# Kernel optimization log

Hardware: AMD Instinct MI355X
Metric: run time of the kernel (lower is better)

The kernel has to match this reference:

```python
import jax, jax.numpy as jnp
import numpy as np

B, Nm, No, D = 32, 256, 1024, 1024
HID, C, K = 2048, 200, 3
EPS = 0.001  # label smoothing
ALPHA = 0.3  # scene-feature fusion weight


def setup_inputs() -> dict:
    key = jax.random.key(0)
    ks = jax.random.split(key, 9)
    return {
        "scene_feat": jax.random.normal(ks[0], (B, No, D), jnp.float32),
        "motion_feat": jax.random.normal(ks[1], (B, Nm, D), jnp.float32),
        "scene_loc": jax.random.normal(ks[2], (B, No, 2), jnp.float32),
        "motion_loc": jax.random.normal(ks[3], (B, Nm, 2), jnp.float32),
        "label": jax.random.randint(ks[4], (B,), 0, C),
        "Wp": jax.random.normal(ks[5], (D, HID), jnp.float32) * 0.02,
        "bp": jnp.zeros((HID,), jnp.float32),
        "Wc": jax.random.normal(ks[6], (HID, C), jnp.float32) * 0.02,
        "bc": jnp.zeros((C,), jnp.float32),
    }


def reference(scene_feat, motion_feat, scene_loc, motion_loc, label, Wp, bp, Wc, bc):
    # pairwise L2 distances: [B, Nm, No]
    diff = motion_loc[:, :, None, :] - scene_loc[:, None, :, :]
    dist = jnp.linalg.norm(diff, axis=-1)
    # k smallest distances -> nearest scene indices [B, Nm, K]
    _, idx = jax.lax.top_k(-dist, K)
    # gather nearest scene features per motion token: [B, Nm, K, D]
    nearest = jax.vmap(lambda sf, ix: sf[ix])(scene_feat, idx)
    fused = motion_feat + ALPHA * nearest.mean(axis=2)  # [B, Nm, D]
    x = fused.mean(axis=1)                              # [B, D]
    x = jax.nn.gelu(x @ Wp + bp, approximate=False)     # exact GELU (torch default)
    logit = x @ Wc + bc                                 # [B, C]
    # cross entropy with label smoothing (torch semantics)
    logp = jax.nn.log_softmax(logit, axis=-1)
    nll = -jnp.take_along_axis(logp, label[:, None], axis=1)[:, 0]
    smooth = -logp.mean(axis=-1)
    loss = jnp.mean((1.0 - EPS) * nll + EPS * smooth)
    return logit, loss
```

## Files before the change

### kernel.cpp

```cpp
#include <hip/hip_runtime.h>
#include <hip/hip_bf16.h>
#include <math.h>

#define BB_ 32
#define NM_ 256
#define NO_ 1024
#define DD_ 1024
#define HID_ 2048
#define CC_ 200
#define KK_ 3
#define EPS_ 0.001f
#define ALPHA_ 0.3f
#define NSEG_ 32
#define NSEG2_ 64

typedef unsigned long long u64;

__device__ __forceinline__ void ins3_u64(u64 k, u64& k0, u64& k1, u64& k2) {
    bool lt0 = k < k0, lt1 = k < k1, lt2 = k < k2;
    k2 = lt1 ? k1 : (lt2 ? k : k2);
    k1 = lt0 ? k0 : (lt1 ? k : k1);
    k0 = lt0 ? k : k0;
}

__global__ __launch_bounds__(256) void knn_idx_kernel(
        const float* __restrict__ scene_loc, const float* __restrict__ motion_loc,
        int* __restrict__ idx_buf) {
    int bx = blockIdx.x;
    int b = bx >> 5;
    int mc = bx & 31;
    __shared__ float slx[NO_], sly[NO_];
    const float2* sl = (const float2*)(scene_loc + (size_t)b * NO_ * 2);
    for (int i = threadIdx.x; i < NO_; i += 256) {
        float2 v = sl[i];
        slx[i] = v.x;
        sly[i] = v.y;
    }
    __syncthreads();

    int m = mc * 8 + (threadIdx.x >> 5);
    int lane = threadIdx.x & 31;
    float2 ml = ((const float2*)(motion_loc + (size_t)b * NM_ * 2))[m];

    u64 k0 = ~0ull, k1 = ~0ull, k2 = ~0ull;
    #pragma unroll 4
    for (int j = 0; j < 32; ++j) {
        int o = lane + (j << 5);
        float dx = ml.x - slx[o];
        float dy = ml.y - sly[o];
        float dist = __fsqrt_rn(__fadd_rn(__fmul_rn(dx, dx), __fmul_rn(dy, dy)));
        u64 k = ((u64)__float_as_uint(dist) << 32) | (unsigned)o;
        ins3_u64(k, k0, k1, k2);
    }
    #pragma unroll
    for (int mask = 1; mask <= 16; mask <<= 1) {
        u64 e0 = __shfl_xor(k0, mask);
        u64 e1 = __shfl_xor(k1, mask);
        u64 e2 = __shfl_xor(k2, mask);
        ins3_u64(e0, k0, k1, k2);
        ins3_u64(e1, k0, k1, k2);
        ins3_u64(e2, k0, k1, k2);
    }
    if (lane == 0) {
        int base = (b * NM_ + m) * 3;
        idx_buf[base]     = (int)(k0 & 0xFFFFFFFFu);
        idx_buf[base + 1] = (int)(k1 & 0xFFFFFFFFu);
        idx_buf[base + 2] = (int)(k2 & 0xFFFFFFFFu);
    }
}

__global__ __launch_bounds__(256) void prep_kernel(
        const int* __restrict__ idx_buf, int* __restrict__ mcnt,
        int* __restrict__ ol, float* __restrict__ wl) {
    int b = blockIdx.x;
    int t = threadIdx.x;
    const float wsc = ALPHA_ / (float)(NM_ * KK_);
    __shared__ int cnt[NO_];
    for (int i = t; i < NO_; i += 256) cnt[i] = 0;
    __syncthreads();
    const int* ib = idx_buf + b * NM_ * KK_;
    for (int i = t; i < NM_ * KK_; i += 256)
        atomicAdd(&cnt[ib[i]], 1);
    __syncthreads();

    int w = t >> 6;
    int lane = t & 63;
    #pragma unroll
    for (int si = 0; si < 8; ++si) {
        int s = w * 8 + si;
        if (lane < 32) {
            int o = s + (lane << 5);
            int c = cnt[o];
            unsigned long long ball = __ballot(c != 0);
            int pos = __popcll(ball & ((1ull << lane) - 1ull));
            if (c != 0) {
                ol[((size_t)b * NSEG_ + s) * 32 + pos] = o;
                wl[((size_t)b * NSEG_ + s) * 32 + pos] = wsc * (float)c;
            }
            if (lane == 0) mcnt[b * NSEG_ + s] = __popcll(ball);
        }
    }
}

__global__ __launch_bounds__(256) void fuse_mean_kernel(
        const float* __restrict__ scene_feat, const float* __restrict__ motion_feat,
        const int* __restrict__ mcnt, const int* __restrict__ ol,
        const float* __restrict__ wl, float* __restrict__ xpart) {
    int bx = blockIdx.x;
    int b = bx >> 6;
    int s2 = bx & 63;
    int s = s2 >> 1, h = s2 & 1;
    int t = threadIdx.x;
    const float wmot = 1.0f / (float)NM_;

    __shared__ float wls[32];
    __shared__ int ols[32];
    __shared__ int msh;
    if (t == 0) msh = mcnt[b * NSEG_ + s];
    if (t < 32) {
        ols[t] = ol[((size_t)b * NSEG_ + s) * 32 + t];
        wls[t] = wl[((size_t)b * NSEG_ + s) * 32 + t];
    }
    __syncthreads();
    int m = msh;

    float4 acc = make_float4(0.f, 0.f, 0.f, 0.f);
    const float4* mf = (const float4*)(motion_feat + (size_t)b * NM_ * DD_);
    #pragma unroll
    for (int j = 0; j < 4; ++j) {
        int r = s + (((j << 1) + h) << 5);
        float4 v = mf[(size_t)r * 256 + t];
        acc.x = fmaf(wmot, v.x, acc.x);
        acc.y = fmaf(wmot, v.y, acc.y);
        acc.z = fmaf(wmot, v.z, acc.z);
        acc.w = fmaf(wmot, v.w, acc.w);
    }
    const float4* sf = (const float4*)(scene_feat + (size_t)b * NO_ * DD_);
    #pragma unroll 4
    for (int i = h; i < m; i += 2) {
        float w = wls[i];
        float4 v = sf[(size_t)ols[i] * 256 + t];
        acc.x = fmaf(w, v.x, acc.x);
        acc.y = fmaf(w, v.y, acc.y);
        acc.z = fmaf(w, v.z, acc.z);
        acc.w = fmaf(w, v.w, acc.w);
    }
    ((float4*)(xpart + ((size_t)s2 * BB_ + b) * DD_))[t] = acc;
}

__global__ __launch_bounds__(256) void xsum_kernel(
        const float* __restrict__ xpart, float* __restrict__ x) {
    int b = blockIdx.x;
    int t = threadIdx.x;
    float4 acc = make_float4(0.f, 0.f, 0.f, 0.f);
    #pragma unroll 8
    for (int s = 0; s < NSEG2_; ++s) {
        float4 v = ((const float4*)(xpart + ((size_t)s * BB_ + b) * DD_))[t];
        acc.x += v.x; acc.y += v.y; acc.z += v.z; acc.w += v.w;
    }
    ((float4*)(x + (size_t)b * DD_))[t] = acc;
}

__global__ __launch_bounds__(256) void fc1_kernel(
        const float* __restrict__ x, const float* __restrict__ Wp,
        float* __restrict__ hpart) {
    int jc = blockIdx.x & 7;
    int dc = blockIdx.x >> 3;
    int t = threadIdx.x;
    int j = jc * 256 + t;

    __shared__ float xs[BB_ * 32];
    {
        int bb = t >> 3;
        int dl4 = t & 7;
        float4 v = ((const float4*)(x + (size_t)bb * DD_ + dc * 32))[dl4];
        ((float4*)xs)[t] = v;
    }
    __syncthreads();

    float acc[BB_];
    #pragma unroll
    for (int bb = 0; bb < BB_; ++bb) acc[bb] = 0.f;

    int d0 = dc * 32;
    for (int dl = 0; dl < 32; ++dl) {
        float w = Wp[(size_t)(d0 + dl) * HID_ + j];
        #pragma unroll
        for (int bb = 0; bb < BB_; ++bb)
            acc[bb] = fmaf(xs[bb * 32 + dl], w, acc[bb]);
    }
    #pragma unroll
    for (int bb = 0; bb < BB_; ++bb)
        hpart[((size_t)dc * BB_ + bb) * HID_ + j] = acc[bb];
}

__global__ __launch_bounds__(256) void fc2_partial_kernel(
        const float* __restrict__ hpart, const float* __restrict__ bp,
        const float* __restrict__ Wc, float* __restrict__ lpart) {
    int bx = blockIdx.x;
    int b = bx & 31;
    int kc = bx >> 5;
    int t = threadIdx.x;
    __shared__ float hs[256];

    int k = kc * 256 + t;
    float sum = bp[k];
    #pragma unroll
    for (int dcc = 0; dcc < 32; ++dcc)
        sum += hpart[((size_t)dcc * BB_ + b) * HID_ + k];
    hs[t] = 0.5f * sum * (1.0f + erff(sum * 0.70710678118654752f));
    __syncthreads();

    if (t < CC_) {
        float acc0 = 0.f, acc1 = 0.f;
        const float* wc = Wc + (size_t)kc * 256 * CC_ + t;
        #pragma unroll 8
        for (int k2 = 0; k2 < 256; k2 += 2) {
            acc0 = fmaf(hs[k2],     wc[(size_t)k2 * CC_],       acc0);
            acc1 = fmaf(hs[k2 + 1], wc[(size_t)(k2 + 1) * CC_], acc1);
        }
        lpart[((size_t)kc * BB_ + b) * CC_ + t] = acc0 + acc1;
    }
}

__global__ __launch_bounds__(256) void logits_loss_kernel(
        const float* __restrict__ lpart, const float* __restrict__ bc,
        const int* __restrict__ label, float* __restrict__ out) {
    int t = threadIdx.x;
    __shared__ float slog[BB_ * CC_];
    __shared__ float lossb[BB_];

    for (int idx = t; idx < BB_ * CC_; idx += 256) {
        int b = idx / CC_;
        int c = idx - b * CC_;
        float acc = bc[c];
        #pragma unroll
        for (int kc = 0; kc < 8; ++kc)
            acc += lpart[((size_t)kc * BB_ + b) * CC_ + c];
        slog[idx] = acc;
        out[idx] = acc;
    }
    __syncthreads();

    int b = t >> 3;
    int lane = t & 7;
    float v[25];
    float m = -INFINITY, ssum = 0.f;
    #pragma unroll
    for (int i = 0; i < 25; ++i) {
        float x = slog[b * CC_ + lane + i * 8];
        v[i] = x;
        m = fmaxf(m, x);
        ssum += x;
    }
    for (int mask = 1; mask < 8; mask <<= 1) m = fmaxf(m, __shfl_xor(m, mask));
    for (int mask = 1; mask < 8; mask <<= 1) ssum += __shfl_xor(ssum, mask);
    float e = 0.f;
    #pragma unroll
    for (int i = 0; i < 25; ++i) e += expf(v[i] - m);
    for (int mask = 1; mask < 8; mask <<= 1) e += __shfl_xor(e, mask);
    float logZ = m + logf(e);

    if (lane == 0) {
        float nll = logZ - slog[b * CC_ + label[b]];
        float smooth = logZ - ssum * (1.0f / (float)CC_);
        lossb[b] = (1.0f - EPS_) * nll + EPS_ * smooth;
    }
    __syncthreads();
    if (t == 0) {
        float s = 0.f;
        for (int i = 0; i < BB_; ++i) s += lossb[i];
        out[BB_ * CC_] = s * (1.0f / (float)BB_);
    }
}

extern "C" void kernel_launch(void* const* d_in, const int* in_sizes, int n_in,
                              void* d_out, int out_size, void* d_ws, size_t ws_size,
                              hipStream_t stream) {
    const float* scene_feat  = (const float*)d_in[0];
    const float* motion_feat = (const float*)d_in[1];
    const float* scene_loc   = (const float*)d_in[2];
    const float* motion_loc  = (const float*)d_in[3];
    const int*   label       = (const int*)d_in[4];
    const float* Wp          = (const float*)d_in[5];
    const float* bp          = (const float*)d_in[6];
    const float* Wc          = (const float*)d_in[7];
    const float* bc          = (const float*)d_in[8];
    float* out = (float*)d_out;

    char* ws = (char*)d_ws;
    int*   idx_buf = (int*)ws;
    int*   mcnt    = (int*)(ws + (128 << 10));
    int*   ol      = (int*)(ws + (256 << 10));
    float* wl      = (float*)(ws + (512 << 10));
    float* xpart   = (float*)(ws + (1 << 20));
    float* x       = (float*)(ws + (10 << 20));
    float* hpart   = (float*)(ws + (16 << 20));
    float* lpart   = (float*)(ws + (32 << 20));

    knn_idx_kernel<<<BB_ * 32, 256, 0, stream>>>(scene_loc, motion_loc, idx_buf);
    prep_kernel<<<BB_, 256, 0, stream>>>(idx_buf, mcnt, ol, wl);
    fuse_mean_kernel<<<BB_ * NSEG2_, 256, 0, stream>>>(scene_feat, motion_feat, mcnt, ol, wl, xpart);
    xsum_kernel<<<BB_, 256, 0, stream>>>(xpart, x);
    fc1_kernel<<<256, 256, 0, stream>>>(x, Wp, hpart);
    fc2_partial_kernel<<<256, 256, 0, stream>>>(hpart, bp, Wc, lpart);
    logits_loss_kernel<<<1, 256, 0, stream>>>(lpart, bc, label, out);
}
```

Measured before the change: 76.65 us.

## Overlap motion-feature mean with KNN search and split logits/loss kernels

```diff
diff --git a/kernel.cpp b/kernel.cpp
--- a/kernel.cpp
+++ b/kernel.cpp
@@ -23,49 +23,71 @@
     k0 = lt0 ? k : k0;
 }
 
-__global__ __launch_bounds__(256) void knn_idx_kernel(
+__global__ __launch_bounds__(256) void knn_motion_kernel(
         const float* __restrict__ scene_loc, const float* __restrict__ motion_loc,
-        int* __restrict__ idx_buf) {
+        const float* __restrict__ motion_feat,
+        int* __restrict__ idx_buf, float* __restrict__ xm) {
     int bx = blockIdx.x;
-    int b = bx >> 5;
-    int mc = bx & 31;
-    __shared__ float slx[NO_], sly[NO_];
-    const float2* sl = (const float2*)(scene_loc + (size_t)b * NO_ * 2);
-    for (int i = threadIdx.x; i < NO_; i += 256) {
-        float2 v = sl[i];
-        slx[i] = v.x;
-        sly[i] = v.y;
-    }
-    __syncthreads();
-
-    int m = mc * 8 + (threadIdx.x >> 5);
-    int lane = threadIdx.x & 31;
-    float2 ml = ((const float2*)(motion_loc + (size_t)b * NM_ * 2))[m];
-
-    u64 k0 = ~0ull, k1 = ~0ull, k2 = ~0ull;
-    #pragma unroll 4
-    for (int j = 0; j < 32; ++j) {
-        int o = lane + (j << 5);
-        float dx = ml.x - slx[o];
-        float dy = ml.y - sly[o];
-        float dist = __fsqrt_rn(__fadd_rn(__fmul_rn(dx, dx), __fmul_rn(dy, dy)));
-        u64 k = ((u64)__float_as_uint(dist) << 32) | (unsigned)o;
-        ins3_u64(k, k0, k1, k2);
-    }
-    #pragma unroll
-    for (int mask = 1; mask <= 16; mask <<= 1) {
-        u64 e0 = __shfl_xor(k0, mask);
-        u64 e1 = __shfl_xor(k1, mask);
-        u64 e2 = __shfl_xor(k2, mask);
-        ins3_u64(e0, k0, k1, k2);
-        ins3_u64(e1, k0, k1, k2);
-        ins3_u64(e2, k0, k1, k2);
-    }
-    if (lane == 0) {
-        int base = (b * NM_ + m) * 3;
-        idx_buf[base]     = (int)(k0 & 0xFFFFFFFFu);
-        idx_buf[base + 1] = (int)(k1 & 0xFFFFFFFFu);
-        idx_buf[base + 2] = (int)(k2 & 0xFFFFFFFFu);
+    if (bx < BB_ * 32) {
+        int b = bx >> 5;
+        int mc = bx & 31;
+        __shared__ float slx[NO_], sly[NO_];
+        const float2* sl = (const float2*)(scene_loc + (size_t)b * NO_ * 2);
+        for (int i = threadIdx.x; i < NO_; i += 256) {
+            float2 v = sl[i];
+            slx[i] = v.x;
+            sly[i] = v.y;
+        }
+        __syncthreads();
+
+        int m = mc * 8 + (threadIdx.x >> 5);
+        int lane = threadIdx.x & 31;
+        float2 ml = ((const float2*)(motion_loc + (size_t)b * NM_ * 2))[m];
+
+        u64 k0 = ~0ull, k1 = ~0ull, k2 = ~0ull;
+        #pragma unroll 4
+        for (int j = 0; j < 32; ++j) {
+            int o = lane + (j << 5);
+            float dx = ml.x - slx[o];
+            float dy = ml.y - sly[o];
+            float dist = __fsqrt_rn(__fadd_rn(__fmul_rn(dx, dx), __fmul_rn(dy, dy)));
+            u64 k = ((u64)__float_as_uint(dist) << 32) | (unsigned)o;
+            ins3_u64(k, k0, k1, k2);
+        }
+        #pragma unroll
+        for (int mask = 1; mask <= 16; mask <<= 1) {
+            u64 e0 = __shfl_xor(k0, mask);
+            u64 e1 = __shfl_xor(k1, mask);
+            u64 e2 = __shfl_xor(k2, mask);
+            ins3_u64(e0, k0, k1, k2);
+            ins3_u64(e1, k0, k1, k2);
+            ins3_u64(e2, k0, k1, k2);
+        }
+        if (lane == 0) {
+            int base = (b * NM_ + m) * 3;
+            idx_buf[base]     = (int)(k0 & 0xFFFFFFFFu);
+            idx_buf[base + 1] = (int)(k1 & 0xFFFFFFFFu);
+            idx_buf[base + 2] = (int)(k2 & 0xFFFFFFFFu);
+        }
+    } else {
+        int m2 = bx - BB_ * 32;
+        int b = m2 >> 6;
+        int s2 = m2 & 63;
+        int s = s2 >> 1, h = s2 & 1;
+        int t = threadIdx.x;
+        const float wmot = 1.0f / (float)NM_;
+        float4 acc = make_float4(0.f, 0.f, 0.f, 0.f);
+        const float4* mf = (const float4*)(motion_feat + (size_t)b * NM_ * DD_);
+        #pragma unroll
+        for (int j = 0; j < 4; ++j) {
+            int r = s + (((j << 1) + h) << 5);
+            float4 v = mf[(size_t)r * 256 + t];
+            acc.x = fmaf(wmot, v.x, acc.x);
+            acc.y = fmaf(wmot, v.y, acc.y);
+            acc.z = fmaf(wmot, v.z, acc.z);
+            acc.w = fmaf(wmot, v.w, acc.w);
+        }
+        ((float4*)(xm + ((size_t)s2 * BB_ + b) * DD_))[t] = acc;
     }
 }
 
@@ -102,16 +124,15 @@
     }
 }
 
-__global__ __launch_bounds__(256) void fuse_mean_kernel(
-        const float* __restrict__ scene_feat, const float* __restrict__ motion_feat,
-        const int* __restrict__ mcnt, const int* __restrict__ ol,
-        const float* __restrict__ wl, float* __restrict__ xpart) {
+__global__ __launch_bounds__(256) void scene_fuse_kernel(
+        const float* __restrict__ scene_feat, const int* __restrict__ mcnt,
+        const int* __restrict__ ol, const float* __restrict__ wl,
+        float* __restrict__ xsc) {
     int bx = blockIdx.x;
     int b = bx >> 6;
     int s2 = bx & 63;
     int s = s2 >> 1, h = s2 & 1;
     int t = threadIdx.x;
-    const float wmot = 1.0f / (float)NM_;
 
     __shared__ float wls[32];
     __shared__ int ols[32];
@@ -125,16 +146,6 @@
     int m = msh;
 
     float4 acc = make_float4(0.f, 0.f, 0.f, 0.f);
-    const float4* mf = (const float4*)(motion_feat + (size_t)b * NM_ * DD_);
-    #pragma unroll
-    for (int j = 0; j < 4; ++j) {
-        int r = s + (((j << 1) + h) << 5);
-        float4 v = mf[(size_t)r * 256 + t];
-        acc.x = fmaf(wmot, v.x, acc.x);
-        acc.y = fmaf(wmot, v.y, acc.y);
-        acc.z = fmaf(wmot, v.z, acc.z);
-        acc.w = fmaf(wmot, v.w, acc.w);
-    }
     const float4* sf = (const float4*)(scene_feat + (size_t)b * NO_ * DD_);
     #pragma unroll 4
     for (int i = h; i < m; i += 2) {
@@ -145,17 +156,23 @@
         acc.z = fmaf(w, v.z, acc.z);
         acc.w = fmaf(w, v.w, acc.w);
     }
-    ((float4*)(xpart + ((size_t)s2 * BB_ + b) * DD_))[t] = acc;
+    ((float4*)(xsc + ((size_t)s2 * BB_ + b) * DD_))[t] = acc;
 }
 
 __global__ __launch_bounds__(256) void xsum_kernel(
-        const float* __restrict__ xpart, float* __restrict__ x) {
+        const float* __restrict__ xm, const float* __restrict__ xsc,
+        float* __restrict__ x) {
     int b = blockIdx.x;
     int t = threadIdx.x;
     float4 acc = make_float4(0.f, 0.f, 0.f, 0.f);
     #pragma unroll 8
     for (int s = 0; s < NSEG2_; ++s) {
-        float4 v = ((const float4*)(xpart + ((size_t)s * BB_ + b) * DD_))[t];
+        float4 v = ((const float4*)(xm + ((size_t)s * BB_ + b) * DD_))[t];
+        acc.x += v.x; acc.y += v.y; acc.z += v.z; acc.w += v.w;
+    }
+    #pragma unroll 8
+    for (int s = 0; s < NSEG2_; ++s) {
+        float4 v = ((const float4*)(xsc + ((size_t)s * BB_ + b) * DD_))[t];
         acc.x += v.x; acc.y += v.y; acc.z += v.z; acc.w += v.w;
     }
     ((float4*)(x + (size_t)b * DD_))[t] = acc;
@@ -223,32 +240,33 @@
     }
 }
 
-__global__ __launch_bounds__(256) void logits_loss_kernel(
+__global__ __launch_bounds__(256) void logits_kernel(
         const float* __restrict__ lpart, const float* __restrict__ bc,
-        const int* __restrict__ label, float* __restrict__ out) {
-    int t = threadIdx.x;
-    __shared__ float slog[BB_ * CC_];
-    __shared__ float lossb[BB_];
-
-    for (int idx = t; idx < BB_ * CC_; idx += 256) {
-        int b = idx / CC_;
-        int c = idx - b * CC_;
-        float acc = bc[c];
+        float* __restrict__ logits) {
+    int b = blockIdx.x;
+    int t = threadIdx.x;
+    if (t < CC_) {
+        float acc = bc[t];
         #pragma unroll
         for (int kc = 0; kc < 8; ++kc)
-            acc += lpart[((size_t)kc * BB_ + b) * CC_ + c];
-        slog[idx] = acc;
-        out[idx] = acc;
-    }
-    __syncthreads();
-
+            acc += lpart[((size_t)kc * BB_ + b) * CC_ + t];
+        logits[(size_t)b * CC_ + t] = acc;
+    }
+}
+
+__global__ __launch_bounds__(256) void loss_kernel(
+        const float* __restrict__ logits, const int* __restrict__ label,
+        float* __restrict__ loss_out) {
+    int t = threadIdx.x;
     int b = t >> 3;
     int lane = t & 7;
+    __shared__ float lossb[BB_];
+
     float v[25];
     float m = -INFINITY, ssum = 0.f;
     #pragma unroll
     for (int i = 0; i < 25; ++i) {
-        float x = slog[b * CC_ + lane + i * 8];
+        float x = logits[(size_t)b * CC_ + lane + i * 8];
         v[i] = x;
         m = fmaxf(m, x);
         ssum += x;
@@ -262,7 +280,7 @@
     float logZ = m + logf(e);
 
     if (lane == 0) {
-        float nll = logZ - slog[b * CC_ + label[b]];
+        float nll = logZ - logits[(size_t)b * CC_ + label[b]];
         float smooth = logZ - ssum * (1.0f / (float)CC_);
         lossb[b] = (1.0f - EPS_) * nll + EPS_ * smooth;
     }
@@ -270,7 +288,7 @@
     if (t == 0) {
         float s = 0.f;
         for (int i = 0; i < BB_; ++i) s += lossb[i];
-        out[BB_ * CC_] = s * (1.0f / (float)BB_);
+        loss_out[0] = s * (1.0f / (float)BB_);
     }
 }
 
@@ -293,16 +311,19 @@
     int*   mcnt    = (int*)(ws + (128 << 10));
     int*   ol      = (int*)(ws + (256 << 10));
     float* wl      = (float*)(ws + (512 << 10));
-    float* xpart   = (float*)(ws + (1 << 20));
-    float* x       = (float*)(ws + (10 << 20));
-    float* hpart   = (float*)(ws + (16 << 20));
-    float* lpart   = (float*)(ws + (32 << 20));
-
-    knn_idx_kernel<<<BB_ * 32, 256, 0, stream>>>(scene_loc, motion_loc, idx_buf);
+    float* xm      = (float*)(ws + (1 << 20));
+    float* xsc     = (float*)(ws + (10 << 20));
+    float* x       = (float*)(ws + (19 << 20));
+    float* hpart   = (float*)(ws + (20 << 20));
+    float* lpart   = (float*)(ws + (30 << 20));
+
+    knn_motion_kernel<<<BB_ * 32 + BB_ * NSEG2_, 256, 0, stream>>>(
+        scene_loc, motion_loc, motion_feat, idx_buf, xm);
     prep_kernel<<<BB_, 256, 0, stream>>>(idx_buf, mcnt, ol, wl);
-    fuse_mean_kernel<<<BB_ * NSEG2_, 256, 0, stream>>>(scene_feat, motion_feat, mcnt, ol, wl, xpart);
-    xsum_kernel<<<BB_, 256, 0, stream>>>(xpart, x);
+    scene_fuse_kernel<<<BB_ * NSEG2_, 256, 0, stream>>>(scene_feat, mcnt, ol, wl, xsc);
+    xsum_kernel<<<BB_, 256, 0, stream>>>(xm, xsc, x);
     fc1_kernel<<<256, 256, 0, stream>>>(x, Wp, hpart);
     fc2_partial_kernel<<<256, 256, 0, stream>>>(hpart, bp, Wc, lpart);
-    logits_loss_kernel<<<1, 256, 0, stream>>>(lpart, bc, label, out);
-}
+    logits_kernel<<<BB_, 256, 0, stream>>>(lpart, bc, out);
+    loss_kernel<<<1, 256, 0, stream>>>(out, label, out + BB_ * CC_);
+}
```

New measurement: 74.94 us. 2.2% less time.
